# Optimization experiments

Hardware: AMD Instinct MI355X
Metric: run time of the kernel (lower is better)

The kernel has to match this reference:

```python
import jax, jax.numpy as jnp
import numpy as np

NUM_HEADS = 12


def setup_inputs() -> dict:
    key = jax.random.key(0)
    ks = jax.random.split(key, 6)
    B, H, W, C = 8, 32, 32, 768
    nt = 8
    hd = C // NUM_HEADS
    s = 0.02  # init scale so softmax logits stay in a sane range
    return {
        "x": jax.random.normal(ks[0], (B, H, W, C), jnp.float32),
        "visual_prompts": jax.random.normal(ks[1], (B, nt, C), jnp.float32),
        "qkv_w": jax.random.normal(ks[2], (C, 3 * C), jnp.float32) * s,
        "qkv_b": jnp.zeros((3 * C,), jnp.float32),
        "proj_w": jax.random.normal(ks[3], (C, C), jnp.float32) * s,
        "proj_b": jnp.zeros((C,), jnp.float32),
        "rel_pos_h": jax.random.normal(ks[4], (2 * H - 1, hd), jnp.float32) * s,
        "rel_pos_w": jax.random.normal(ks[5], (2 * W - 1, hd), jnp.float32) * s,
    }


def _get_rel_pos(size, rel_pos):
    # q_size == k_size == size, rel_pos already has length 2*size-1 -> pure gather
    coords = jnp.arange(size)[:, None] - jnp.arange(size)[None, :] + (size - 1)
    return rel_pos[coords]  # (size, size, head_dim)


def reference(x, visual_prompts, qkv_w, qkv_b, proj_w, proj_b, rel_pos_h, rel_pos_w):
    B, H, W, C = x.shape
    nh = NUM_HEADS
    hd = C // nh
    nt = visual_prompts.shape[1]
    N = H * W + nt
    scale = hd ** -0.5

    xs = jnp.concatenate([visual_prompts, x.reshape(B, H * W, C)], axis=1)  # (B,N,C)
    qkv = (xs @ qkv_w + qkv_b).reshape(B, N, 3, nh, hd)
    qkv = qkv.transpose(2, 0, 3, 1, 4).reshape(3, B * nh, N, hd)
    q, k, v = qkv[0], qkv[1], qkv[2]  # each (B*nh, N, hd)

    attn = jnp.einsum('bqc,bkc->bqk', q * scale, k)  # (B*nh, N, N)

    # decomposed rel-pos bias on the visual (non-prompt) block
    Rh = _get_rel_pos(H, rel_pos_h)  # (H,H,hd)
    Rw = _get_rel_pos(W, rel_pos_w)  # (W,W,hd)
    r_q = q[:, nt:].reshape(B * nh, H, W, hd)
    rel_h = jnp.einsum('bhwc,hkc->bhwk', r_q, Rh)  # (B*nh,H,W,H)
    rel_w = jnp.einsum('bhwc,wkc->bhwk', r_q, Rw)  # (B*nh,H,W,W)
    bias = (rel_h[..., :, None] + rel_w[..., None, :]).reshape(B * nh, H * W, H * W)
    attn = attn.at[:, nt:, nt:].add(bias)

    # prompt-token mask: visual queries cannot attend to prompt keys (-100 logit)
    attn = attn.at[:, nt:, :nt].add(-100.0)

    attn = jax.nn.softmax(attn, axis=-1)
    out = jnp.einsum('bqk,bkc->bqc', attn, v)  # (B*nh,N,hd)
    out = out.reshape(B, nh, N, hd).transpose(0, 2, 1, 3).reshape(B, N, C)
    out = out @ proj_w + proj_b

    x_out = out[:, nt:].reshape(B, H, W, C)
    vp_out = out[:, :nt]
    return x_out, vp_out
```

## Files before the change

### kernel.cpp

```cpp
#include <hip/hip_runtime.h>
#include <stdint.h>

typedef __attribute__((ext_vector_type(8))) short s8v;
typedef __attribute__((ext_vector_type(4))) short s4v;
typedef __attribute__((ext_vector_type(4))) float f4v;
typedef __attribute__((ext_vector_type(4))) unsigned short us4v;
typedef __attribute__((ext_vector_type(4))) float f32x4v;

#define DEV static __device__ __forceinline__

#define L2E 1.44269504f

DEV unsigned short f2bf(float f){
  uint32_t x = __builtin_bit_cast(uint32_t, f);
  uint32_t r = x + 0x7fffu + ((x >> 16) & 1u);
  return (unsigned short)(r >> 16);
}

DEV float exp2g(float x){
#if __has_builtin(__builtin_amdgcn_exp2f)
  return __builtin_amdgcn_exp2f(x);
#else
  return exp2f(x);
#endif
}

DEV s4v pack4(float a, float b, float c, float d){
  uint32_t r0, r1;
  asm("v_cvt_pk_bf16_f32 %0, %1, %2" : "=v"(r0) : "v"(a), "v"(b));
  asm("v_cvt_pk_bf16_f32 %0, %1, %2" : "=v"(r1) : "v"(c), "v"(d));
  union { uint32_t u[2]; s4v s; } u; u.u[0] = r0; u.u[1] = r1; return u.s;
}

DEV f4v mfma32(s8v a, s8v b, f4v c){
  return __builtin_amdgcn_mfma_f32_16x16x32_bf16(a, b, c, 0, 0, 0);
}
DEV f4v mfma16(s4v a, s4v b, f4v c){
  return __builtin_amdgcn_mfma_f32_16x16x16bf16_1k(a, b, c, 0, 0, 0);
}

DEV void load_lds16(const void* g, void* l){
  __builtin_amdgcn_global_load_lds((const __attribute__((address_space(1))) uint32_t*)g,
                                   (__attribute__((address_space(3))) uint32_t*)l, 16, 0, 0);
}

__global__ __launch_bounds__(256) void k_prep(const float* __restrict__ x,
    const float* __restrict__ vp, const float* __restrict__ qw,
    const float* __restrict__ pw, unsigned short* __restrict__ xs,
    unsigned short* __restrict__ Wt, unsigned short* __restrict__ Pt){
  __shared__ float tile[32][33];
  const int bid = blockIdx.x;
  if (bid < 6192){
    int64_t e = ((int64_t)bid * 256 + threadIdx.x) * 4;
    int m = (int)(e / 768); int c = (int)(e % 768);
    int b = m / 1032, n = m % 1032;
    const float* src = (n < 8) ? (vp + ((int64_t)(b * 8 + n)) * 768 + c)
                               : (x  + ((int64_t)(b * 1024 + (n - 8))) * 768 + c);
    f32x4v v = *(const f32x4v*)src;
    us4v o = { f2bf(v[0]), f2bf(v[1]), f2bf(v[2]), f2bf(v[3]) };
    *(us4v*)(xs + e) = o;
    return;
  }
  const int wb = bid - 6192;
  const float* src; unsigned short* dst; int Cc, j0, k0;
  if (wb < 1728){
    int jt = wb % 72, kt = wb / 72;
    src = qw; dst = Wt; Cc = 2304; k0 = kt * 32; j0 = jt * 32;
  } else {
    int t2 = wb - 1728;
    int jt = t2 % 24, kt = t2 / 24;
    src = pw; dst = Pt; Cc = 768; k0 = kt * 32; j0 = jt * 32;
  }
  const int t = threadIdx.x;
  const int r = t >> 3, c4 = (t & 7) * 4;
  f32x4v v = *(const f32x4v*)(src + (int64_t)(k0 + r) * Cc + j0 + c4);
  tile[r][c4 + 0] = v[0]; tile[r][c4 + 1] = v[1];
  tile[r][c4 + 2] = v[2]; tile[r][c4 + 3] = v[3];
  __syncthreads();
  us4v o = { f2bf(tile[c4 + 0][r]), f2bf(tile[c4 + 1][r]),
             f2bf(tile[c4 + 2][r]), f2bf(tile[c4 + 3][r]) };
  *(us4v*)(dst + (int64_t)(j0 + r) * 768 + k0 + c4) = o;
}

template<int MODE>
__global__ __launch_bounds__(256) void k_gemm(
    const unsigned short* __restrict__ A, const unsigned short* __restrict__ Bt,
    const float* __restrict__ bias, int M, int N, int K,
    unsigned short* __restrict__ qb, unsigned short* __restrict__ kb,
    unsigned short* __restrict__ vtb, float* __restrict__ outp)
{
  __shared__ __align__(16) unsigned short At [128 * 32];
  __shared__ __align__(16) unsigned short Btl[128 * 32];
  const int tid = threadIdx.x, lane = tid & 63, wid = tid >> 6;
  const int mbase = blockIdx.y * 128, nbase = blockIdx.x * 128;
  const int wr = wid >> 1, wc = wid & 1;
  const int g = lane >> 4, l15 = lane & 15;
  const int l2 = lane >> 2, l3 = lane & 3;
  f4v acc[4][4] = {};

  int srow0 = wid * 16 + l2;
  int srow1 = 64 + wid * 16 + l2;
  int sg0 = l3 ^ ((srow0 >> 1) & 3);
  int sg1 = l3 ^ ((srow1 >> 1) & 3);
  int arow0 = mbase + srow0; if (arow0 >= M) arow0 = 0;
  int arow1 = mbase + srow1; if (arow1 >= M) arow1 = 0;
  const unsigned short* a0 = A  + (int64_t)arow0 * K + sg0 * 8;
  const unsigned short* a1 = A  + (int64_t)arow1 * K + sg1 * 8;
  const unsigned short* b0 = Bt + (int64_t)(nbase + srow0) * K + sg0 * 8;
  const unsigned short* b1 = Bt + (int64_t)(nbase + srow1) * K + sg1 * 8;
  unsigned short* lA0 = At  + wid * 16 * 32;
  unsigned short* lA1 = At  + (64 + wid * 16) * 32;
  unsigned short* lB0 = Btl + wid * 16 * 32;
  unsigned short* lB1 = Btl + (64 + wid * 16) * 32;

  for (int ks = 0; ks < K; ks += 32){
    load_lds16(a0 + ks, lA0);
    load_lds16(a1 + ks, lA1);
    load_lds16(b0 + ks, lB0);
    load_lds16(b1 + ks, lB1);
    __syncthreads();
    s8v af[4], bf[4];
    #pragma unroll
    for (int mc = 0; mc < 4; mc++){
      int row = wr * 64 + mc * 16 + l15;
      int o = (row * 64 + g * 16) ^ (((row >> 1) & 3) << 4);
      af[mc] = *(const s8v*)((const char*)At + o);
    }
    #pragma unroll
    for (int nc = 0; nc < 4; nc++){
      int row = wc * 64 + nc * 16 + l15;
      int o = (row * 64 + g * 16) ^ (((row >> 1) & 3) << 4);
      bf[nc] = *(const s8v*)((const char*)Btl + o);
    }
    #pragma unroll
    for (int mc = 0; mc < 4; mc++)
      #pragma unroll
      for (int nc = 0; nc < 4; nc++)
        acc[mc][nc] = mfma32(af[mc], bf[nc], acc[mc][nc]);
    __syncthreads();
  }

  if (MODE == 0){
    const int which = nbase / 768;
    const int head  = ((nbase % 768) >> 6) + wc;
    #pragma unroll
    for (int nc = 0; nc < 4; nc++){
      int j = nbase + wc * 64 + nc * 16 + l15;
      float bv = bias[j];
      int d = nc * 16 + l15;
      #pragma unroll
      for (int mc = 0; mc < 4; mc++){
        int m0 = mbase + wr * 64 + mc * 16 + g * 4;
        if (m0 >= M) continue;
        int b = m0 / 1032, n = m0 % 1032;
        int bh = b * 12 + head;
        if (which == 2){
          us4v pk = { f2bf(acc[mc][nc][0] + bv), f2bf(acc[mc][nc][1] + bv),
                      f2bf(acc[mc][nc][2] + bv), f2bf(acc[mc][nc][3] + bv) };
          *(us4v*)(vtb + ((int64_t)bh * 64 + d) * 1032 + n) = pk;
        } else {
          unsigned short* dst = (which == 0 ? qb : kb) + ((int64_t)bh * 1032 + n) * 64 + d;
          #pragma unroll
          for (int r = 0; r < 4; r++) dst[(int64_t)r * 64] = f2bf(acc[mc][nc][r] + bv);
        }
      }
    }
  } else {
    #pragma unroll
    for (int nc = 0; nc < 4; nc++){
      int j = nbase + wc * 64 + nc * 16 + l15;
      float bv = bias[j];
      #pragma unroll
      for (int mc = 0; mc < 4; mc++){
        int m0 = mbase + wr * 64 + mc * 16 + g * 4;
        if (m0 >= M) continue;
        int b = m0 / 1032, n0 = m0 % 1032;
        #pragma unroll
        for (int r = 0; r < 4; r++){
          int n = n0 + r;
          float v = acc[mc][nc][r] + bv;
          int64_t dst = (n < 8) ? (6291456LL + ((int64_t)(b * 8 + n)) * 768 + j)
                                : (((int64_t)(b * 1024 + (n - 8))) * 768 + j);
          outp[dst] = v;
        }
      }
    }
  }
}

__global__ __launch_bounds__(64) void k_rel(const unsigned short* __restrict__ qbuf,
    const float* __restrict__ rph, const float* __restrict__ rpw,
    float* __restrict__ relh, float* __restrict__ relw)
{
  const int lane = threadIdx.x;
  const int g = lane >> 4, l15 = lane & 15;
  if (blockIdx.x < 3072){
    const int bh = blockIdx.x >> 5;
    const int qh = blockIdx.x & 31;
    s8v qf[2][2];
    #pragma unroll
    for (int qc = 0; qc < 2; qc++){
      int n = qh * 32 + qc * 16 + l15 + 8;
      #pragma unroll
      for (int ch = 0; ch < 2; ch++)
        qf[qc][ch] = *(const s8v*)(qbuf + ((int64_t)bh * 1032 + n) * 64 + ch * 32 + g * 8);
    }
    s8v rf[2][2];
    #pragma unroll
    for (int kc = 0; kc < 2; kc++){
      int kh = kc * 16 + l15;
      #pragma unroll
      for (int ch = 0; ch < 2; ch++){
        const float* rp = rph + (int64_t)(qh - kh + 31) * 64 + ch * 32 + g * 8;
        f32x4v v0 = *(const f32x4v*)rp;
        f32x4v v1 = *(const f32x4v*)(rp + 4);
        s8v t = { (short)f2bf(v0[0]), (short)f2bf(v0[1]), (short)f2bf(v0[2]), (short)f2bf(v0[3]),
                  (short)f2bf(v1[0]), (short)f2bf(v1[1]), (short)f2bf(v1[2]), (short)f2bf(v1[3]) };
        rf[kc][ch] = t;
      }
    }
    #pragma unroll
    for (int kc = 0; kc < 2; kc++)
      #pragma unroll
      for (int qc = 0; qc < 2; qc++){
        f4v d = {0.f, 0.f, 0.f, 0.f};
        d = mfma32(rf[kc][0], qf[qc][0], d);
        d = mfma32(rf[kc][1], qf[qc][1], d);
        #pragma unroll
        for (int r = 0; r < 4; r++)
          relh[((int64_t)bh * 32 + kc * 16 + g * 4 + r) * 1024 + qh * 32 + qc * 16 + l15] = d[r] * L2E;
      }
  } else {
    const int bid = blockIdx.x - 3072;
    const int bh = bid >> 5;
    const int qw = bid & 31;
    s8v qf[2][2];
    #pragma unroll
    for (int qc = 0; qc < 2; qc++){
      int qp = qw + 32 * (qc * 16 + l15);
      int n = qp + 8;
      #pragma unroll
      for (int ch = 0; ch < 2; ch++)
        qf[qc][ch] = *(const s8v*)(qbuf + ((int64_t)bh * 1032 + n) * 64 + ch * 32 + g * 8);
    }
    s8v wf[2][2];
    #pragma unroll
    for (int kc = 0; kc < 2; kc++){
      int kw = kc * 16 + l15;
      #pragma unroll
      for (int ch = 0; ch < 2; ch++){
        const float* rp = rpw + (int64_t)(qw - kw + 31) * 64 + ch * 32 + g * 8;
        f32x4v v0 = *(const f32x4v*)rp;
        f32x4v v1 = *(const f32x4v*)(rp + 4);
        s8v t = { (short)f2bf(v0[0]), (short)f2bf(v0[1]), (short)f2bf(v0[2]), (short)f2bf(v0[3]),
                  (short)f2bf(v1[0]), (short)f2bf(v1[1]), (short)f2bf(v1[2]), (short)f2bf(v1[3]) };
        wf[kc][ch] = t;
      }
    }
    #pragma unroll
    for (int qc = 0; qc < 2; qc++)
      #pragma unroll
      for (int kc = 0; kc < 2; kc++){
        f4v d = {0.f, 0.f, 0.f, 0.f};
        d = mfma32(qf[qc][0], wf[kc][0], d);
        d = mfma32(qf[qc][1], wf[kc][1], d);
        #pragma unroll
        for (int r = 0; r < 4; r++){
          int qp = qw + 32 * (qc * 16 + g * 4 + r);
          relw[((int64_t)bh * 1024 + qp) * 32 + kc * 16 + l15] = d[r] * L2E;
        }
      }
  }
}

__global__ __launch_bounds__(256, 3) void k_attn(
    const unsigned short* __restrict__ qb, const unsigned short* __restrict__ kb,
    const unsigned short* __restrict__ vtb, const float* __restrict__ relh,
    const float* __restrict__ relw, unsigned short* __restrict__ ao)
{
  const int lane = threadIdx.x & 63, wid = threadIdx.x >> 6;
  const int wq = (blockIdx.x & 7) * 108 + (blockIdx.x >> 3);
  const int bh = wq / 9;
  const int qg = wq % 9;
  int qt = qg * 4 + wid; if (qt > 32) qt = 32;
  const int qbase = qt * 32;
  const int g = lane >> 4, l15 = lane & 15;
  const int b = bh / 12, head = bh % 12;
  const float C1 = 0.125f * L2E;
  const float NEG = -144.269504f;

  __shared__ __align__(16) unsigned short Kl[32 * 64];
  __shared__ __align__(16) unsigned short Vl[64 * 32];

  f4v of[4][2] = {};
  float lrun[2] = {0.f, 0.f};
  int qn_[2], qp_[2];

  s8v qf[2][2];
  float rw[2][2][4];
  #pragma unroll
  for (int qc = 0; qc < 2; qc++){
    int qn = qbase + qc * 16 + l15;
    qn_[qc] = qn;
    int qcl = qn < 1032 ? qn : 1031;
    #pragma unroll
    for (int ch = 0; ch < 2; ch++)
      qf[qc][ch] = *(const s8v*)(qb + ((int64_t)bh * 1032 + qcl) * 64 + ch * 32 + g * 8);
    int qp = qn - 8; if (qp < 0) qp = 0; if (qp > 1023) qp = 1023;
    qp_[qc] = qp;
  }
  #pragma unroll
  for (int qc = 0; qc < 2; qc++)
    #pragma unroll
    for (int kc = 0; kc < 2; kc++)
      #pragma unroll
      for (int r = 0; r < 4; r++){
        int kw = (kc * 16 + g * 4 + r + 24) & 31;
        rw[qc][kc][r] = relw[((int64_t)bh * 1024 + qp_[qc]) * 32 + kw];
      }

  const char* kbb = (const char*)(kb + (int64_t)bh * 1032 * 64);
  const char* vbb = (const char*)(vtb + (int64_t)bh * 64 * 1032);
  const float* rhbase = relh + (int64_t)bh * 32 * 1024;

  const int krow_l = (lane >> 3);
  const int kcol_s = ((lane & 7) ^ krow_l) << 4;
  const int vd_l   = (lane >> 2);
  const int vslot  = ((lane & 3) ^ ((lane >> 2) ^ (lane >> 4)) & 3);
  char* kdst = (char*)Kl + wid * 1024;
  char* vdst = (char*)Vl + wid * 1024;
  const int vsw = (l15 ^ (l15 >> 2)) & 3;

  for (int kt = 0; kt < 33; kt++){
    {
      int gr = kt * 32 + wid * 8 + krow_l; if (gr > 1031) gr = 1031;
      load_lds16(kbb + (int64_t)gr * 128 + kcol_s, kdst);
      int d = wid * 16 + vd_l;
      int scol = kt * 64 + (vslot << 4); if (scol > 2048) scol = 2048;
      load_lds16(vbb + (int64_t)d * 2064 + scol, vdst);
    }
    __syncthreads();

    s8v kf[2][2];
    #pragma unroll
    for (int kc = 0; kc < 2; kc++){
      int roff = (kc * 16 + l15) << 7;
      #pragma unroll
      for (int ch = 0; ch < 2; ch++)
        kf[kc][ch] = *(const s8v*)((const char*)Kl + roff + ((((ch << 2) + g) ^ (l15 & 7)) << 4));
    }
    s4v vf[4][2];
    #pragma unroll
    for (int dc = 0; dc < 4; dc++){
      int doff = ((dc * 16 + l15) << 6) + ((g & 1) << 3);
      #pragma unroll
      for (int kc = 0; kc < 2; kc++)
        vf[dc][kc] = *(const s4v*)((const char*)Vl + doff + ((((kc << 1) + (g >> 1)) ^ vsw) << 4));
    }
    int khA = kt - 1; if (khA < 0) khA = 0;
    int khB = kt; if (khB > 31) khB = 31;
    float rhA[2], rhB[2];
    #pragma unroll
    for (int qc = 0; qc < 2; qc++){
      rhA[qc] = rhbase[(int64_t)khA * 1024 + qp_[qc]];
      rhB[qc] = rhbase[(int64_t)khB * 1024 + qp_[qc]];
    }

    f4v sv[2][2];
    #pragma unroll
    for (int qc = 0; qc < 2; qc++)
      #pragma unroll
      for (int kc = 0; kc < 2; kc++){
        f4v s = {0.f, 0.f, 0.f, 0.f};
        s = mfma32(kf[kc][0], qf[qc][0], s);
        s = mfma32(kf[kc][1], qf[qc][1], s);
        sv[qc][kc] = s;
      }

    const bool anyprompt = (kt == 0);
    const bool anymask = (kt == 32);
    s4v bp[2][2];
    #pragma unroll
    for (int qc = 0; qc < 2; qc++){
      const bool qpr = qn_[qc] < 8;
      float p[8];
      #pragma unroll
      for (int kc = 0; kc < 2; kc++)
        #pragma unroll
        for (int r = 0; r < 4; r++){
          int off = kc * 16 + g * 4 + r;
          float bias = qpr ? 0.f : ((off >= 8 ? rhB[qc] : rhA[qc]) + rw[qc][kc][r]);
          if (anyprompt && off < 8 && !qpr) bias = NEG;
          float L = fmaf(sv[qc][kc][r], C1, bias);
          if (anymask && off >= 8) L = NEG;
          p[kc * 4 + r] = exp2g(L);
        }
      lrun[qc] += ((p[0]+p[1])+(p[2]+p[3])) + ((p[4]+p[5])+(p[6]+p[7]));
      bp[qc][0] = pack4(p[0], p[1], p[2], p[3]);
      bp[qc][1] = pack4(p[4], p[5], p[6], p[7]);
    }
    #pragma unroll
    for (int dc = 0; dc < 4; dc++)
      #pragma unroll
      for (int kc = 0; kc < 2; kc++)
        #pragma unroll
        for (int qc = 0; qc < 2; qc++)
          of[dc][qc] = mfma16(vf[dc][kc], bp[qc][kc], of[dc][qc]);

    __syncthreads();
  }

  #pragma unroll
  for (int qc = 0; qc < 2; qc++){
    int qn = qn_[qc];
    if (qn >= 1032) continue;
    float lt = lrun[qc];
    lt += __shfl_xor(lt, 16);
    lt += __shfl_xor(lt, 32);
    float inv = 1.0f / lt;
    unsigned short* dst = ao + ((int64_t)(b * 1032 + qn)) * 768 + head * 64;
    #pragma unroll
    for (int dc = 0; dc < 4; dc++){
      us4v pk = { f2bf(of[dc][qc][0] * inv), f2bf(of[dc][qc][1] * inv),
                  f2bf(of[dc][qc][2] * inv), f2bf(of[dc][qc][3] * inv) };
      *(us4v*)(dst + dc * 16 + g * 4) = pk;
    }
  }
}

extern "C" void kernel_launch(void* const* d_in, const int* in_sizes, int n_in,
                              void* d_out, int out_size, void* d_ws, size_t ws_size,
                              hipStream_t stream)
{
  const float* x   = (const float*)d_in[0];
  const float* vp  = (const float*)d_in[1];
  const float* qw  = (const float*)d_in[2];
  const float* qbb = (const float*)d_in[3];
  const float* pw  = (const float*)d_in[4];
  const float* pb  = (const float*)d_in[5];
  const float* rph = (const float*)d_in[6];
  const float* rpw = (const float*)d_in[7];
  float* out = (float*)d_out;

  char* ws = (char*)d_ws;
  size_t off = 0;
  auto alloc = [&](size_t bytes) -> void* {
    void* p = ws + off;
    off = (off + bytes + 255) & ~(size_t)255;
    return p;
  };
  unsigned short* xs   = (unsigned short*)alloc((size_t)8256 * 768 * 2);
  unsigned short* Wt   = (unsigned short*)alloc((size_t)2304 * 768 * 2);
  unsigned short* Pt   = (unsigned short*)alloc((size_t)768 * 768 * 2);
  unsigned short* qbuf = (unsigned short*)alloc((size_t)96 * 1032 * 64 * 2);
  unsigned short* kbuf = (unsigned short*)alloc((size_t)96 * 1032 * 64 * 2 + 4096);
  unsigned short* vtb  = (unsigned short*)alloc((size_t)96 * 64 * 1032 * 2 + 4096);
  float* relh = (float*)alloc((size_t)96 * 32 * 1024 * 4);
  float* relw = (float*)alloc((size_t)96 * 1024 * 32 * 4);
  unsigned short* ao = xs;

  k_prep<<<8496, 256, 0, stream>>>(x, vp, qw, pw, xs, Wt, Pt);
  k_gemm<0><<<dim3(18, 65), 256, 0, stream>>>(xs, Wt, qbb, 8256, 2304, 768,
                                              qbuf, kbuf, vtb, nullptr);
  k_rel<<<6144, 64, 0, stream>>>(qbuf, rph, rpw, relh, relw);
  k_attn<<<864, 256, 0, stream>>>(qbuf, kbuf, vtb, relh, relw, ao);
  k_gemm<1><<<dim3(6, 65), 256, 0, stream>>>(ao, Pt, pb, 8256, 768, 768,
                                             nullptr, nullptr, nullptr, out);
}
```

Before: 168.6 us.

## Split attention key range across two wave groups and remap GEMM blocks per XCD

The attention kernel now runs 512 threads per block. Two groups of four waves each process half of the key tiles (17 and 16) for the same queries, and the partial outputs and row sums are merged through shared memory at the end. This shortens the serial key loop per wave and raises parallelism, at the cost of extra LDS, a merge step, and an idle iteration for the second group. Separately, the GEMM block index is remapped so that consecutive tiles land on the same XCD, which should improve L2 locality.

```diff
diff --git a/kernel.cpp b/kernel.cpp
--- a/kernel.cpp
+++ b/kernel.cpp
@@ -92,7 +92,12 @@
   __shared__ __align__(16) unsigned short At [128 * 32];
   __shared__ __align__(16) unsigned short Btl[128 * 32];
   const int tid = threadIdx.x, lane = tid & 63, wid = tid >> 6;
-  const int mbase = blockIdx.y * 128, nbase = blockIdx.x * 128;
+  const int nbx = gridDim.x, nwg = nbx * gridDim.y;
+  const int bid = blockIdx.y * nbx + blockIdx.x;
+  const int xcd = bid & 7, idx = bid >> 3;
+  const int q8 = nwg >> 3, r8 = nwg & 7;
+  const int wgid = (xcd < r8 ? xcd * (q8 + 1) : r8 * (q8 + 1) + (xcd - r8) * q8) + idx;
+  const int mbase = (wgid / nbx) * 128, nbase = (wgid % nbx) * 128;
   const int wr = wid >> 1, wc = wid & 1;
   const int g = lane >> 4, l15 = lane & 15;
   const int l2 = lane >> 2, l3 = lane & 3;
@@ -273,24 +278,27 @@
   }
 }
 
-__global__ __launch_bounds__(256, 3) void k_attn(
+__global__ __launch_bounds__(512, 4) void k_attn(
     const unsigned short* __restrict__ qb, const unsigned short* __restrict__ kb,
     const unsigned short* __restrict__ vtb, const float* __restrict__ relh,
     const float* __restrict__ relw, unsigned short* __restrict__ ao)
 {
   const int lane = threadIdx.x & 63, wid = threadIdx.x >> 6;
+  const int qtl = wid & 3, h = wid >> 2;
   const int wq = (blockIdx.x & 7) * 108 + (blockIdx.x >> 3);
   const int bh = wq / 9;
   const int qg = wq % 9;
-  int qt = qg * 4 + wid; if (qt > 32) qt = 32;
+  int qt = qg * 4 + qtl; if (qt > 32) qt = 32;
   const int qbase = qt * 32;
   const int g = lane >> 4, l15 = lane & 15;
   const int b = bh / 12, head = bh % 12;
   const float C1 = 0.125f * L2E;
   const float NEG = -144.269504f;
 
-  __shared__ __align__(16) unsigned short Kl[32 * 64];
-  __shared__ __align__(16) unsigned short Vl[64 * 32];
+  __shared__ __align__(16) unsigned short Kl[2][32 * 64];
+  __shared__ __align__(16) unsigned short Vl[2][64 * 32];
+  __shared__ __align__(16) float ofs[4][4][2][64][4];
+  __shared__ float lsh[4][2][64];
 
   f4v of[4][2] = {};
   float lrun[2] = {0.f, 0.f};
@@ -327,103 +335,124 @@
   const int kcol_s = ((lane & 7) ^ krow_l) << 4;
   const int vd_l   = (lane >> 2);
   const int vslot  = ((lane & 3) ^ ((lane >> 2) ^ (lane >> 4)) & 3);
-  char* kdst = (char*)Kl + wid * 1024;
-  char* vdst = (char*)Vl + wid * 1024;
+  char* kdst = (char*)Kl[h] + qtl * 1024;
+  char* vdst = (char*)Vl[h] + qtl * 1024;
   const int vsw = (l15 ^ (l15 >> 2)) & 3;
 
-  for (int kt = 0; kt < 33; kt++){
-    {
-      int gr = kt * 32 + wid * 8 + krow_l; if (gr > 1031) gr = 1031;
+  const int ktbase = h ? 17 : 0;
+  const int ntile  = h ? 16 : 17;
+
+  for (int i = 0; i < 17; i++){
+    const bool act = (i < ntile);
+    const int kt = ktbase + i;
+    if (act){
+      int gr = kt * 32 + qtl * 8 + krow_l; if (gr > 1031) gr = 1031;
       load_lds16(kbb + (int64_t)gr * 128 + kcol_s, kdst);
-      int d = wid * 16 + vd_l;
+      int d = qtl * 16 + vd_l;
       int scol = kt * 64 + (vslot << 4); if (scol > 2048) scol = 2048;
       load_lds16(vbb + (int64_t)d * 2064 + scol, vdst);
     }
     __syncthreads();
 
-    s8v kf[2][2];
-    #pragma unroll
-    for (int kc = 0; kc < 2; kc++){
-      int roff = (kc * 16 + l15) << 7;
-      #pragma unroll
-      for (int ch = 0; ch < 2; ch++)
-        kf[kc][ch] = *(const s8v*)((const char*)Kl + roff + ((((ch << 2) + g) ^ (l15 & 7)) << 4));
-    }
-    s4v vf[4][2];
-    #pragma unroll
-    for (int dc = 0; dc < 4; dc++){
-      int doff = ((dc * 16 + l15) << 6) + ((g & 1) << 3);
-      #pragma unroll
-      for (int kc = 0; kc < 2; kc++)
-        vf[dc][kc] = *(const s4v*)((const char*)Vl + doff + ((((kc << 1) + (g >> 1)) ^ vsw) << 4));
-    }
-    int khA = kt - 1; if (khA < 0) khA = 0;
-    int khB = kt; if (khB > 31) khB = 31;
-    float rhA[2], rhB[2];
+    if (act){
+      const char* Kc = (const char*)Kl[h];
+      const char* Vc = (const char*)Vl[h];
+      s8v kf[2][2];
+      #pragma unroll
+      for (int kc = 0; kc < 2; kc++){
+        int roff = (kc * 16 + l15) << 7;
+        #pragma unroll
+        for (int ch = 0; ch < 2; ch++)
+          kf[kc][ch] = *(const s8v*)(Kc + roff + ((((ch << 2) + g) ^ (l15 & 7)) << 4));
+      }
+      s4v vf[4][2];
+      #pragma unroll
+      for (int dc = 0; dc < 4; dc++){
+        int doff = ((dc * 16 + l15) << 6) + ((g & 1) << 3);
+        #pragma unroll
+        for (int kc = 0; kc < 2; kc++)
+          vf[dc][kc] = *(const s4v*)(Vc + doff + ((((kc << 1) + (g >> 1)) ^ vsw) << 4));
+      }
+      int khA = kt - 1; if (khA < 0) khA = 0;
+      int khB = kt; if (khB > 31) khB = 31;
+      float rhA[2], rhB[2];
+      #pragma unroll
+      for (int qc = 0; qc < 2; qc++){
+        rhA[qc] = rhbase[(int64_t)khA * 1024 + qp_[qc]];
+        rhB[qc] = rhbase[(int64_t)khB * 1024 + qp_[qc]];
+      }
+      f4v sv[2][2];
+      #pragma unroll
+      for (int qc = 0; qc < 2; qc++)
+        #pragma unroll
+        for (int kc = 0; kc < 2; kc++){
+          f4v s = {0.f, 0.f, 0.f, 0.f};
+          s = mfma32(kf[kc][0], qf[qc][0], s);
+          s = mfma32(kf[kc][1], qf[qc][1], s);
+          sv[qc][kc] = s;
+        }
+      const bool anyprompt = (kt == 0);
+      const bool anymask = (kt == 32);
+      s4v bp[2][2];
+      #pragma unroll
+      for (int qc = 0; qc < 2; qc++){
+        const bool qpr = qn_[qc] < 8;
+        float p[8];
+        #pragma unroll
+        for (int kc = 0; kc < 2; kc++)
+          #pragma unroll
+          for (int r = 0; r < 4; r++){
+            int off = kc * 16 + g * 4 + r;
+            float bias = qpr ? 0.f : ((off >= 8 ? rhB[qc] : rhA[qc]) + rw[qc][kc][r]);
+            if (anyprompt && off < 8 && !qpr) bias = NEG;
+            float L = fmaf(sv[qc][kc][r], C1, bias);
+            if (anymask && off >= 8) L = NEG;
+            p[kc * 4 + r] = exp2g(L);
+          }
+        lrun[qc] += ((p[0]+p[1])+(p[2]+p[3])) + ((p[4]+p[5])+(p[6]+p[7]));
+        bp[qc][0] = pack4(p[0], p[1], p[2], p[3]);
+        bp[qc][1] = pack4(p[4], p[5], p[6], p[7]);
+      }
+      #pragma unroll
+      for (int dc = 0; dc < 4; dc++)
+        #pragma unroll
+        for (int kc = 0; kc < 2; kc++)
+          #pragma unroll
+          for (int qc = 0; qc < 2; qc++)
+            of[dc][qc] = mfma16(vf[dc][kc], bp[qc][kc], of[dc][qc]);
+    }
+
+    __syncthreads();
+  }
+
+  if (h == 1){
+    #pragma unroll
+    for (int dc = 0; dc < 4; dc++)
+      #pragma unroll
+      for (int qc = 0; qc < 2; qc++)
+        *(f4v*)&ofs[qtl][dc][qc][lane][0] = of[dc][qc];
+    #pragma unroll
+    for (int qc = 0; qc < 2; qc++)
+      lsh[qtl][qc][lane] = lrun[qc];
+  }
+  __syncthreads();
+  if (h == 0){
     #pragma unroll
     for (int qc = 0; qc < 2; qc++){
-      rhA[qc] = rhbase[(int64_t)khA * 1024 + qp_[qc]];
-      rhB[qc] = rhbase[(int64_t)khB * 1024 + qp_[qc]];
-    }
-
-    f4v sv[2][2];
-    #pragma unroll
-    for (int qc = 0; qc < 2; qc++)
-      #pragma unroll
-      for (int kc = 0; kc < 2; kc++){
-        f4v s = {0.f, 0.f, 0.f, 0.f};
-        s = mfma32(kf[kc][0], qf[qc][0], s);
-        s = mfma32(kf[kc][1], qf[qc][1], s);
-        sv[qc][kc] = s;
-      }
-
-    const bool anyprompt = (kt == 0);
-    const bool anymask = (kt == 32);
-    s4v bp[2][2];
-    #pragma unroll
-    for (int qc = 0; qc < 2; qc++){
-      const bool qpr = qn_[qc] < 8;
-      float p[8];
-      #pragma unroll
-      for (int kc = 0; kc < 2; kc++)
-        #pragma unroll
-        for (int r = 0; r < 4; r++){
-          int off = kc * 16 + g * 4 + r;
-          float bias = qpr ? 0.f : ((off >= 8 ? rhB[qc] : rhA[qc]) + rw[qc][kc][r]);
-          if (anyprompt && off < 8 && !qpr) bias = NEG;
-          float L = fmaf(sv[qc][kc][r], C1, bias);
-          if (anymask && off >= 8) L = NEG;
-          p[kc * 4 + r] = exp2g(L);
-        }
-      lrun[qc] += ((p[0]+p[1])+(p[2]+p[3])) + ((p[4]+p[5])+(p[6]+p[7]));
-      bp[qc][0] = pack4(p[0], p[1], p[2], p[3]);
-      bp[qc][1] = pack4(p[4], p[5], p[6], p[7]);
-    }
-    #pragma unroll
-    for (int dc = 0; dc < 4; dc++)
-      #pragma unroll
-      for (int kc = 0; kc < 2; kc++)
-        #pragma unroll
-        for (int qc = 0; qc < 2; qc++)
-          of[dc][qc] = mfma16(vf[dc][kc], bp[qc][kc], of[dc][qc]);
-
-    __syncthreads();
-  }
-
-  #pragma unroll
-  for (int qc = 0; qc < 2; qc++){
-    int qn = qn_[qc];
-    if (qn >= 1032) continue;
-    float lt = lrun[qc];
-    lt += __shfl_xor(lt, 16);
-    lt += __shfl_xor(lt, 32);
-    float inv = 1.0f / lt;
-    unsigned short* dst = ao + ((int64_t)(b * 1032 + qn)) * 768 + head * 64;
-    #pragma unroll
-    for (int dc = 0; dc < 4; dc++){
-      us4v pk = { f2bf(of[dc][qc][0] * inv), f2bf(of[dc][qc][1] * inv),
-                  f2bf(of[dc][qc][2] * inv), f2bf(of[dc][qc][3] * inv) };
-      *(us4v*)(dst + dc * 16 + g * 4) = pk;
+      int qn = qn_[qc];
+      if (qn >= 1032) continue;
+      float lt = lrun[qc] + lsh[qtl][qc][lane];
+      lt += __shfl_xor(lt, 16);
+      lt += __shfl_xor(lt, 32);
+      float inv = 1.0f / lt;
+      unsigned short* dst = ao + ((int64_t)(b * 1032 + qn)) * 768 + head * 64;
+      #pragma unroll
+      for (int dc = 0; dc < 4; dc++){
+        f4v ot = of[dc][qc] + *(const f4v*)&ofs[qtl][dc][qc][lane][0];
+        us4v pk = { f2bf(ot[0] * inv), f2bf(ot[1] * inv),
+                    f2bf(ot[2] * inv), f2bf(ot[3] * inv) };
+        *(us4v*)(dst + dc * 16 + g * 4) = pk;
+      }
     }
   }
 }
@@ -463,7 +492,7 @@
   k_gemm<0><<<dim3(18, 65), 256, 0, stream>>>(xs, Wt, qbb, 8256, 2304, 768,
                                               qbuf, kbuf, vtb, nullptr);
   k_rel<<<6144, 64, 0, stream>>>(qbuf, rph, rpw, relh, relw);
-  k_attn<<<864, 256, 0, stream>>>(qbuf, kbuf, vtb, relh, relw, ao);
+  k_attn<<<864, 512, 0, stream>>>(qbuf, kbuf, vtb, relh, relw, ao);
   k_gemm<1><<<dim3(6, 65), 256, 0, stream>>>(ao, Pt, pb, 8256, 768, 768,
                                              nullptr, nullptr, nullptr, out);
 }
```

New measurement: 176.5 us. +4.7%, slower.
